# Kernel tuning notes

Hardware: AMD Instinct MI355X
Metric: run time of the kernel (lower is better)

## Reference

```python
import jax, jax.numpy as jnp
import numpy as np
import math

N, D = 4096, 1024

def setup_inputs() -> dict:
    key = jax.random.key(0)
    ks = jax.random.split(key, 12)
    x = jax.random.normal(ks[0], (N, D), dtype=jnp.float32)
    attention_mask = jax.random.randint(ks[1], (N, N), 0, 2).astype(jnp.float32)
    learnable_mask = jax.random.randint(ks[2], (N, N), 0, 2).astype(jnp.float32)
    boundary_mask = jax.random.randint(ks[3], (N, 1), 0, 2).astype(jnp.float32)
    s = 1.0 / math.sqrt(D)
    W_q = jax.random.normal(ks[4], (D, D), dtype=jnp.float32) * s
    b_q = jax.random.normal(ks[5], (D,), dtype=jnp.float32) * s
    W_k = jax.random.normal(ks[6], (D, D), dtype=jnp.float32) * s
    b_k = jax.random.normal(ks[7], (D,), dtype=jnp.float32) * s
    W_v = jax.random.normal(ks[8], (D, D), dtype=jnp.float32) * s
    b_v = jax.random.normal(ks[9], (D,), dtype=jnp.float32) * s
    connection = jax.random.normal(ks[10], (D, D), dtype=jnp.float32) * s
    bias = jnp.ones((1,), dtype=jnp.float32) * 0.01
    return {"x": x, "attention_mask": attention_mask, "learnable_mask": learnable_mask,
            "boundary_mask": boundary_mask, "W_q": W_q, "b_q": b_q, "W_k": W_k, "b_k": b_k,
            "W_v": W_v, "b_v": b_v, "connection": connection, "bias": bias}

def reference(x, attention_mask, learnable_mask, boundary_mask,
              W_q, b_q, W_k, b_k, W_v, b_v, connection, bias):
    # Linear layers (torch Linear: x @ W.T + b)
    q = x @ W_q.T + b_q            # [N, D]
    k = x @ W_k.T + b_k            # [N, D]
    v = x @ W_v.T + b_v            # [N, D]
    d_head = k.shape[-1]
    attention_logits = (q @ k.T) / jnp.sqrt(jnp.asarray(d_head, x.dtype))  # [N, N]
    connection_logits = (q @ connection) @ k.T + bias                      # [N, N]
    # straight-through hard sigmoid mask
    soft_mask = jax.nn.sigmoid(connection_logits)
    st_mask = (soft_mask > 0.5).astype(x.dtype) - jax.lax.stop_gradient(soft_mask) + soft_mask
    lm = st_mask * learnable_mask
    mask = attention_mask + lm
    mask = -10000.0 * (1.0 - mask)
    attention = jax.nn.softmax(attention_logits + mask, axis=-1)  # [N, N]
    x_residual = attention @ v                                    # [N, D]
    out = boundary_mask * x_residual + (1.0 - boundary_mask) * x
    return out
```

## Files before the change

### kernel.cpp

```cpp
#include <hip/hip_runtime.h>
#include <cstdint>


typedef __attribute__((ext_vector_type(8))) short short8;
typedef __attribute__((ext_vector_type(4))) float f32x4;
typedef __attribute__((ext_vector_type(4))) float f4v;
typedef __attribute__((ext_vector_type(4))) unsigned short u16x4;
typedef __attribute__((ext_vector_type(8))) unsigned short u16x8;

typedef unsigned short u16;
typedef unsigned char u8;

__device__ __forceinline__ u16 f2bf(float f) {
  unsigned u = __float_as_uint(f);
  u += 0x7fffu + ((u >> 16) & 1u);
  return (u16)(u >> 16);
}
__device__ __forceinline__ float bf2f(u16 h) {
  return __uint_as_float(((unsigned)h) << 16);
}

__device__ __forceinline__ void gld16(void* lds, const void* g) {
  __builtin_amdgcn_global_load_lds(
      (__attribute__((address_space(1))) void*)g,
      (__attribute__((address_space(3))) void*)lds,
      16, 0, 0);
}


__global__ void prep_x(const float* __restrict__ x, u16* __restrict__ xs3) {
  int id = blockIdx.x * 256 + threadIdx.x;
  int flat = id * 4;
  int n = flat >> 10, i = flat & 1023;
  f4v v = *(const f4v*)(x + (size_t)flat);
  u16x4 hi, lo;
#pragma unroll
  for (int e = 0; e < 4; e++) {
    float f = v[e];
    u16 h = f2bf(f);
    hi[e] = h;
    lo[e] = f2bf(f - bf2f(h));
  }
  size_t base = (size_t)n * 3072 + i;
  *(u16x4*)(xs3 + base) = hi;
  *(u16x4*)(xs3 + base + 1024) = lo;
  *(u16x4*)(xs3 + base + 2048) = hi;
}

__global__ void prep_w(const float* __restrict__ Wq, const float* __restrict__ Wk,
                       const float* __restrict__ Wv, u16* __restrict__ W3) {
  int id = blockIdx.x * 256 + threadIdx.x;
  int flat = id * 4;
  int o = flat >> 10, i = flat & 1023;
  const float* src = (o < 1024) ? (Wq + (size_t)o * 1024)
                   : (o < 2048) ? (Wk + (size_t)(o - 1024) * 1024)
                                : (Wv + (size_t)(o - 2048) * 1024);
  f4v v = *(const f4v*)(src + i);
  u16x4 hi, lo;
#pragma unroll
  for (int e = 0; e < 4; e++) {
    u16 h = f2bf(v[e]);
    hi[e] = h;
    lo[e] = f2bf(v[e] - bf2f(h));
  }
  size_t base = (size_t)o * 3072 + i;
  *(u16x4*)(W3 + base) = hi;
  *(u16x4*)(W3 + base + 1024) = hi;
  *(u16x4*)(W3 + base + 2048) = lo;
}

__global__ void prep_bias(const float* __restrict__ bq, const float* __restrict__ bk,
                          const float* __restrict__ bv, float* __restrict__ bp) {
  int id = blockIdx.x * 256 + threadIdx.x;
  float v = (id < 1024) ? bq[id] : (id < 2048) ? bk[id - 1024] : bv[id - 2048];
  bp[id] = v;
}

__global__ void prep_c(const float* __restrict__ C, u16* __restrict__ C3) {
  __shared__ float t[32][33];
  int lx = threadIdx.x & 31, ly = threadIdx.x >> 5;
  int i0 = blockIdx.x * 32, j0 = blockIdx.y * 32;
#pragma unroll
  for (int r = 0; r < 32; r += 8)
    t[ly + r][lx] = C[(size_t)(i0 + ly + r) * 1024 + j0 + lx];
  __syncthreads();
#pragma unroll
  for (int r = 0; r < 32; r += 8) {
    float f = t[lx][ly + r];
    u16 h = f2bf(f);
    u16 l = f2bf(f - bf2f(h));
    size_t o = (size_t)(j0 + ly + r) * 3072 + i0 + lx;
    C3[o] = h;
    C3[o + 1024] = h;
    C3[o + 2048] = l;
  }
}


struct EpiG1 {
  const float* bp; u16* qs3; u16* k3; u16* vt; int mode;
  __device__ void operator()(int r, int c, float v) const {
    if (mode == 0) {
      v += bp[c];
      u16 h = f2bf(v);
      u16 l = f2bf(v - bf2f(h));
      if (c < 1024) {
        size_t b = (size_t)r * 3072 + c;
        qs3[b] = h; qs3[b + 1024] = l; qs3[b + 2048] = h;
      } else {
        size_t b = (size_t)r * 3072 + (c - 1024);
        k3[b] = h; k3[b + 1024] = h; k3[b + 2048] = l;
      }
    } else {
      v += bp[2048 + r];
      vt[(size_t)r * 4096 + c] = f2bf(v);
    }
  }
};

struct EpiQCS {
  u16* qc3; u16* Sc; int isS;
  __device__ void operator()(int r, int c, float v) const {
    if (isS) {
      Sc[(size_t)r * 4096 + c] = f2bf(v);
    } else {
      u16 h = f2bf(v);
      u16 l = f2bf(v - bf2f(h));
      size_t b = (size_t)r * 3072 + c;
      qc3[b] = h; qc3[b + 1024] = l; qc3[b + 2048] = h;
    }
  }
};

struct EpiCL {
  u8* st; float b0;
  __device__ void operator()(int r, int c, float v) const {
    st[(size_t)r * 4096 + c] = (v + b0 > 0.f) ? 1 : 0;
  }
};

struct EpiPart {
  float* part;
  __device__ void operator()(int r, int c, float v) const {
    part[(size_t)r * 1024 + c] = v;
  }
};

template <class Epi>
__device__ __forceinline__ void gemm_core(
    const u16* __restrict__ A, const u16* __restrict__ B,
    int lda, int ldb, int K, int mBase, int nBase, Epi epi) {
  __shared__ __align__(16) u16 lA[128 * 64];
  __shared__ __align__(16) u16 lB[128 * 64];
  const int tid = threadIdx.x;
  const int wave = tid >> 6, lane = tid & 63;
  const int wm = wave & 1, wn = wave >> 1;
  const int lane16 = lane & 15, quad = lane >> 4;

  const int srow = tid >> 3;
  const int gchunk = ((tid & 7) ^ (srow & 7)) * 8;
  const u16* aP = A + (size_t)(mBase + srow) * lda + gchunk;
  const u16* bP = B + (size_t)(nBase + srow) * ldb + gchunk;
  const int woff = wave * 1024;

  const int rsw = lane16 & 7;
  const u16* raB = lA + (wm * 64 + lane16) * 64;
  const u16* rbB = lB + (wn * 64 + lane16) * 64;

  f32x4 acc[4][4];
#pragma unroll
  for (int i = 0; i < 4; i++)
#pragma unroll
    for (int j = 0; j < 4; j++) acc[i][j] = (f32x4){0.f, 0.f, 0.f, 0.f};

  for (int k0 = 0; k0 < K; k0 += 64) {
#pragma unroll
    for (int i = 0; i < 4; i++) {
      gld16((char*)lA + i * 4096 + woff, aP + (size_t)(32 * i) * lda + k0);
      gld16((char*)lB + i * 4096 + woff, bP + (size_t)(32 * i) * ldb + k0);
    }
    __syncthreads();
    short8 af[2][4], bfr[2][4];
#pragma unroll
    for (int s = 0; s < 2; s++) {
      const int sl = (((s << 2) + quad) ^ rsw) * 8;
#pragma unroll
      for (int j = 0; j < 4; j++) {
        af[s][j]  = *(const short8*)(raB + j * 1024 + sl);
        bfr[s][j] = *(const short8*)(rbB + j * 1024 + sl);
      }
    }
#pragma unroll
    for (int s = 0; s < 2; s++)
#pragma unroll
      for (int im = 0; im < 4; im++)
#pragma unroll
        for (int in = 0; in < 4; in++)
          acc[im][in] = __builtin_amdgcn_mfma_f32_16x16x32_bf16(
              af[s][im], bfr[s][in], acc[im][in], 0, 0, 0);
    __syncthreads();
  }

#pragma unroll
  for (int im = 0; im < 4; im++)
#pragma unroll
    for (int in = 0; in < 4; in++)
#pragma unroll
      for (int i = 0; i < 4; i++) {
        int r = mBase + wm * 64 + im * 16 + quad * 4 + i;
        int c = nBase + wn * 64 + in * 16 + lane16;
        epi(r, c, acc[im][in][i]);
      }
}

__global__ __launch_bounds__(256, 2) void gemm_g1(
    const u16* __restrict__ xs3, const u16* __restrict__ W3,
    const float* __restrict__ bp, u16* __restrict__ qs3,
    u16* __restrict__ k3, u16* __restrict__ vt) {
  const int bid = blockIdx.x;
  if (bid < 512) {
    gemm_core(xs3, W3, 3072, 3072, 3072, (bid >> 4) * 128, (bid & 15) * 128,
              EpiG1{bp, qs3, k3, vt, 0});
  } else {
    const int t = bid - 512;
    gemm_core(W3 + (size_t)2048 * 3072, xs3, 3072, 3072, 1024,
              (t & 7) * 128, (t >> 3) * 128, EpiG1{bp, qs3, k3, vt, 1});
  }
}

__global__ __launch_bounds__(256, 2) void gemm_qc_s(
    const u16* __restrict__ qs3, const u16* __restrict__ C3,
    const u16* __restrict__ k3, u16* __restrict__ qc3, u16* __restrict__ Sc) {
  const int bid = blockIdx.x;
  if (bid < 256) {
    gemm_core(qs3, C3, 3072, 3072, 3072, (bid >> 3) * 128, (bid & 7) * 128,
              EpiQCS{qc3, Sc, 0});
  } else {
    const int t = bid - 256;
    gemm_core(qs3, k3, 3072, 3072, 1024, (t >> 5) * 128, (t & 31) * 128,
              EpiQCS{qc3, Sc, 1});
  }
}

__global__ __launch_bounds__(256, 2) void gemm_cl(
    const u16* __restrict__ qc3, const u16* __restrict__ k3,
    const float* __restrict__ bias, u8* __restrict__ st) {
  gemm_core(qc3, k3, 3072, 3072, 3072, blockIdx.y * 128, blockIdx.x * 128,
            EpiCL{st, bias[0]});
}

__global__ __launch_bounds__(256, 2) void gemm_pv(
    const u16* __restrict__ P, const u16* __restrict__ vt,
    float* __restrict__ parts) {
  const size_t kOff = (size_t)blockIdx.z * 2048;
  gemm_core(P + kOff, vt + kOff, 4096, 4096, 2048,
            blockIdx.y * 128, blockIdx.x * 128,
            EpiPart{parts + (size_t)blockIdx.z * 4096 * 1024});
}

__global__ void reduce_out(const float* __restrict__ x, const float* __restrict__ bm,
                           const float* __restrict__ parts, float* __restrict__ out) {
  int id = blockIdx.x * 256 + threadIdx.x;
  int flat = id * 4;
  int r = flat >> 10;
  float b = bm[r];
  f4v xv = *(const f4v*)(x + (size_t)flat);
  f4v p0 = *(const f4v*)(parts + (size_t)flat);
  f4v p1 = *(const f4v*)(parts + (size_t)4096 * 1024 + flat);
  f4v o;
#pragma unroll
  for (int e = 0; e < 4; e++) o[e] = b * (p0[e] + p1[e]) + (1.0f - b) * xv[e];
  *(f4v*)(out + (size_t)flat) = o;
}

__global__ __launch_bounds__(256) void mask_softmax(
    const u16* __restrict__ Sc, const u8* __restrict__ st,
    const float* __restrict__ am, const float* __restrict__ lm,
    u16* __restrict__ P) {
  const int n = blockIdx.x, tid = threadIdx.x;
  const int lane = tid & 63, wave = tid >> 6;
  const u16* Srow = Sc + (size_t)n * 4096;
  const u8* Trow = st + (size_t)n * 4096;
  const float* Arow = am + (size_t)n * 4096;
  const float* Lrow = lm + (size_t)n * 4096;

  float lg[16];
  float mx = -3.4e38f;
#pragma unroll
  for (int j = 0; j < 2; j++) {
    int base = (tid + 256 * j) * 8;
    u16x8 s8 = *(const u16x8*)(Srow + base);
    unsigned long long t8 = *(const unsigned long long*)(Trow + base);
    f4v a0 = *(const f4v*)(Arow + base), a1 = *(const f4v*)(Arow + base + 4);
    f4v l0 = *(const f4v*)(Lrow + base), l1 = *(const f4v*)(Lrow + base + 4);
#pragma unroll
    for (int e = 0; e < 8; e++) {
      float stv = ((t8 >> (8 * e)) & 1ull) ? 1.f : 0.f;
      float a = (e < 4) ? a0[e] : a1[e - 4];
      float l = (e < 4) ? l0[e] : l1[e - 4];
      float mv = a + stv * l;
      float v = bf2f(s8[e]) * 0.03125f - 10000.f * (1.f - mv);
      lg[j * 8 + e] = v;
      mx = fmaxf(mx, v);
    }
  }
#pragma unroll
  for (int o = 32; o; o >>= 1) mx = fmaxf(mx, __shfl_xor(mx, o));
  __shared__ float smax[4], ssum[4];
  if (lane == 0) smax[wave] = mx;
  __syncthreads();
  mx = fmaxf(fmaxf(smax[0], smax[1]), fmaxf(smax[2], smax[3]));

  float sum = 0.f;
#pragma unroll
  for (int i = 0; i < 16; i++) { lg[i] = __expf(lg[i] - mx); sum += lg[i]; }
#pragma unroll
  for (int o = 32; o; o >>= 1) sum += __shfl_xor(sum, o);
  if (lane == 0) ssum[wave] = sum;
  __syncthreads();
  float inv = 1.f / (ssum[0] + ssum[1] + ssum[2] + ssum[3]);

  u16* Pr = P + (size_t)n * 4096;
#pragma unroll
  for (int j = 0; j < 2; j++) {
    int base = (tid + 256 * j) * 8;
    u16x8 o8;
#pragma unroll
    for (int e = 0; e < 8; e++) o8[e] = f2bf(lg[j * 8 + e] * inv);
    *(u16x8*)(Pr + base) = o8;
  }
}


extern "C" void kernel_launch(void* const* d_in, const int* in_sizes, int n_in,
                              void* d_out, int out_size, void* d_ws, size_t ws_size,
                              hipStream_t stream) {
  const float* x    = (const float*)d_in[0];
  const float* am   = (const float*)d_in[1];
  const float* lm   = (const float*)d_in[2];
  const float* bm   = (const float*)d_in[3];
  const float* Wq   = (const float*)d_in[4];
  const float* bq   = (const float*)d_in[5];
  const float* Wk   = (const float*)d_in[6];
  const float* bk   = (const float*)d_in[7];
  const float* Wv   = (const float*)d_in[8];
  const float* bv   = (const float*)d_in[9];
  const float* Cc   = (const float*)d_in[10];
  const float* bias = (const float*)d_in[11];
  float* out = (float*)d_out;
  char* ws = (char*)d_ws;

  if (ws_size < 0xB010000) return;

  u16*  xs3 = (u16*) (ws + 0x0000000);
  u16*  W3  = (u16*) (ws + 0x1800000);
  u16*  C3  = (u16*) (ws + 0x2A00000);
  float* bp = (float*)(ws + 0x3000000);
  u16*  qs3 = (u16*) (ws + 0x3010000);
  u16*  qc3 = (u16*) (ws + 0x4810000);
  u16*  k3  = (u16*) (ws + 0x6010000);
  u16*  vt  = (u16*) (ws + 0x7810000);
  u16*  Sc  = (u16*) (ws + 0x8010000);
  u8*   st  = (u8*)  (ws + 0xA010000);
  u16*  P   = (u16*) (ws + 0x0000000);
  float* parts = (float*)(ws + 0x4810000);

  prep_x   <<<4096, 256, 0, stream>>>(x, xs3);
  prep_w   <<<3072, 256, 0, stream>>>(Wq, Wk, Wv, W3);
  prep_bias<<<12,   256, 0, stream>>>(bq, bk, bv, bp);
  prep_c   <<<dim3(32, 32), 256, 0, stream>>>(Cc, C3);

  gemm_g1<<<768, 256, 0, stream>>>(xs3, W3, bp, qs3, k3, vt);
  gemm_qc_s<<<1280, 256, 0, stream>>>(qs3, C3, k3, qc3, Sc);
  gemm_cl<<<dim3(32, 32), 256, 0, stream>>>(qc3, k3, bias, st);
  mask_softmax<<<4096, 256, 0, stream>>>(Sc, st, am, lm, P);
  gemm_pv<<<dim3(8, 32, 2), 256, 0, stream>>>(P, vt, parts);
  reduce_out<<<4096, 256, 0, stream>>>(x, bm, parts, out);
}
```

Measured before the change: 486.9 us.

## Use 256x256 tile GEMM with 4-stage pipeline for connection-logit and PV GEMMs

Adds a 512-thread GEMM core with 256x256 output tiles, a 4-deep LDS ring buffer and explicit waitcnt/barrier scheduling, and uses it for the connection-logits GEMM and the attention-times-V GEMM. The goal is more operand reuse per byte loaded and better overlap of global loads with MFMA work. Block indices are remapped for cache locality. The PV GEMM is split-K into four parts so it still fills the device, which means reduce_out now sums four fp32 partials and moves more memory. The larger tile uses more LDS and registers per block, which may cut occupancy.

```diff
diff --git a/kernel.cpp b/kernel.cpp
--- a/kernel.cpp
+++ b/kernel.cpp
@@ -213,6 +213,111 @@
       }
 }
 
+
+template <class Epi>
+__device__ __forceinline__ void gemm256_core(
+    const u16* __restrict__ A, const u16* __restrict__ B,
+    int lda, int ldb, int K, int mBase, int nBase, Epi epi) {
+  __shared__ __align__(16) u16 lA[4][256 * 32];
+  __shared__ __align__(16) u16 lB[4][256 * 32];
+  const int tid  = threadIdx.x;
+  const int wave = tid >> 6, lane = tid & 63;
+  const int lane16 = lane & 15, quad = lane >> 4;
+  const int wm = wave >> 2, wn = wave & 3;
+  const int NT = K >> 5;
+
+  const int srow = tid >> 2;
+  const int gch  = ((tid & 3) ^ ((tid >> 3) & 3)) * 8;
+  const u16* aS = A + (size_t)(mBase + srow) * lda + gch;
+  const u16* bS = B + (size_t)(nBase + srow) * ldb + gch;
+  const size_t aStep = (size_t)128 * lda, bStep = (size_t)128 * ldb;
+  const int ldsW = wave * 1024;
+
+  const int sw   = (lane16 >> 1) & 3;
+  const int aOff = (wm * 128 + lane16) * 64 + ((quad ^ sw) * 16);
+  const int bOff = (wn * 64  + lane16) * 64 + ((quad ^ sw) * 16);
+
+  f32x4 acc[8][4];
+#pragma unroll
+  for (int j = 0; j < 8; j++)
+#pragma unroll
+    for (int n = 0; n < 4; n++) acc[j][n] = (f32x4){0.f, 0.f, 0.f, 0.f};
+
+  short8 af[8], bfr[4];
+
+  auto stage = [&](int t) {
+    const int bb = (t & 3) * 16384;
+    const size_t kk = (size_t)(t << 5);
+#pragma unroll
+    for (int i = 0; i < 2; i++) {
+      gld16((char*)lA + bb + i * 8192 + ldsW, aS + (size_t)i * aStep + kk);
+      gld16((char*)lB + bb + i * 8192 + ldsW, bS + (size_t)i * bStep + kk);
+    }
+  };
+  auto rdfrags = [&](int t) {
+    const char* la = (const char*)lA + (t & 3) * 16384 + aOff;
+    const char* lb = (const char*)lB + (t & 3) * 16384 + bOff;
+#pragma unroll
+    for (int j = 0; j < 8; j++) af[j] = *(const short8*)(la + j * 1024);
+#pragma unroll
+    for (int n = 0; n < 4; n++) bfr[n] = *(const short8*)(lb + n * 1024);
+  };
+  auto mfma32 = [&]() {
+    __builtin_amdgcn_s_setprio(1);
+#pragma unroll
+    for (int j = 0; j < 8; j++)
+#pragma unroll
+      for (int n = 0; n < 4; n++)
+        acc[j][n] = __builtin_amdgcn_mfma_f32_16x16x32_bf16(
+            af[j], bfr[n], acc[j][n], 0, 0, 0);
+    __builtin_amdgcn_s_setprio(0);
+  };
+
+  stage(0); stage(1); stage(2);
+  asm volatile("s_waitcnt vmcnt(8)" ::: "memory");
+  __builtin_amdgcn_sched_barrier(0);
+  __builtin_amdgcn_s_barrier();
+  __builtin_amdgcn_sched_barrier(0);
+
+  int t = 0;
+  for (; t + 4 <= NT; ++t) {
+    rdfrags(t);
+    stage(t + 3);
+    asm volatile("s_waitcnt vmcnt(8) lgkmcnt(0)" ::: "memory");
+    __builtin_amdgcn_sched_barrier(0);
+    __builtin_amdgcn_s_barrier();
+    __builtin_amdgcn_sched_barrier(0);
+    mfma32();
+  }
+  rdfrags(t);
+  asm volatile("s_waitcnt vmcnt(4) lgkmcnt(0)" ::: "memory");
+  __builtin_amdgcn_sched_barrier(0);
+  __builtin_amdgcn_s_barrier();
+  __builtin_amdgcn_sched_barrier(0);
+  mfma32();
+  ++t;
+  rdfrags(t);
+  asm volatile("s_waitcnt vmcnt(0) lgkmcnt(0)" ::: "memory");
+  __builtin_amdgcn_sched_barrier(0);
+  __builtin_amdgcn_s_barrier();
+  __builtin_amdgcn_sched_barrier(0);
+  mfma32();
+  ++t;
+  rdfrags(t);
+  asm volatile("s_waitcnt lgkmcnt(0)" ::: "memory");
+  __builtin_amdgcn_sched_barrier(0);
+  mfma32();
+
+#pragma unroll
+  for (int j = 0; j < 8; j++)
+#pragma unroll
+    for (int n = 0; n < 4; n++)
+#pragma unroll
+      for (int i = 0; i < 4; i++)
+        epi(mBase + wm * 128 + j * 16 + quad * 4 + i,
+            nBase + wn * 64 + n * 16 + lane16, acc[j][n][i]);
+}
+
 __global__ __launch_bounds__(256, 2) void gemm_g1(
     const u16* __restrict__ xs3, const u16* __restrict__ W3,
     const float* __restrict__ bp, u16* __restrict__ qs3,
@@ -242,34 +347,43 @@
   }
 }
 
-__global__ __launch_bounds__(256, 2) void gemm_cl(
+__global__ __launch_bounds__(512, 2) void gemm_cl256(
     const u16* __restrict__ qc3, const u16* __restrict__ k3,
     const float* __restrict__ bias, u8* __restrict__ st) {
-  gemm_core(qc3, k3, 3072, 3072, 3072, blockIdx.y * 128, blockIdx.x * 128,
-            EpiCL{st, bias[0]});
-}
-
-__global__ __launch_bounds__(256, 2) void gemm_pv(
+  const int bid = blockIdx.x;
+  const int wg = (bid & 7) * 32 + (bid >> 3);
+  gemm256_core(qc3, k3, 3072, 3072, 3072, (wg >> 4) * 256, (wg & 15) * 256,
+               EpiCL{st, bias[0]});
+}
+
+__global__ __launch_bounds__(512, 2) void gemm_pv256(
     const u16* __restrict__ P, const u16* __restrict__ vt,
-    float* __restrict__ parts) {
-  const size_t kOff = (size_t)blockIdx.z * 2048;
-  gemm_core(P + kOff, vt + kOff, 4096, 4096, 2048,
-            blockIdx.y * 128, blockIdx.x * 128,
-            EpiPart{parts + (size_t)blockIdx.z * 4096 * 1024});
+    float* __restrict__ p01, float* __restrict__ p23) {
+  const int bid = blockIdx.x;
+  const int z = bid >> 6, rem = bid & 63;
+  float* base = ((z < 2) ? p01 : p23) + (size_t)(z & 1) * (4096ull * 1024ull);
+  const size_t kOff = (size_t)z * 1024;
+  gemm256_core(P + kOff, vt + kOff, 4096, 4096, 1024,
+               (rem >> 2) * 256, (rem & 3) * 256, EpiPart{base});
 }
 
 __global__ void reduce_out(const float* __restrict__ x, const float* __restrict__ bm,
-                           const float* __restrict__ parts, float* __restrict__ out) {
+                           const float* __restrict__ p01, const float* __restrict__ p23,
+                           float* __restrict__ out) {
   int id = blockIdx.x * 256 + threadIdx.x;
   int flat = id * 4;
   int r = flat >> 10;
   float b = bm[r];
+  const size_t SL = (size_t)4096 * 1024;
   f4v xv = *(const f4v*)(x + (size_t)flat);
-  f4v p0 = *(const f4v*)(parts + (size_t)flat);
-  f4v p1 = *(const f4v*)(parts + (size_t)4096 * 1024 + flat);
+  f4v a0 = *(const f4v*)(p01 + (size_t)flat);
+  f4v a1 = *(const f4v*)(p01 + SL + flat);
+  f4v a2 = *(const f4v*)(p23 + (size_t)flat);
+  f4v a3 = *(const f4v*)(p23 + SL + flat);
   f4v o;
 #pragma unroll
-  for (int e = 0; e < 4; e++) o[e] = b * (p0[e] + p1[e]) + (1.0f - b) * xv[e];
+  for (int e = 0; e < 4; e++)
+    o[e] = b * ((a0[e] + a1[e]) + (a2[e] + a3[e])) + (1.0f - b) * xv[e];
   *(f4v*)(out + (size_t)flat) = o;
 }
 
@@ -363,7 +477,8 @@
   u16*  Sc  = (u16*) (ws + 0x8010000);
   u8*   st  = (u8*)  (ws + 0xA010000);
   u16*  P   = (u16*) (ws + 0x0000000);
-  float* parts = (float*)(ws + 0x4810000);
+  float* parts01 = (float*)(ws + 0x4810000);
+  float* parts23 = (float*)(ws + 0x8010000);
 
   prep_x   <<<4096, 256, 0, stream>>>(x, xs3);
   prep_w   <<<3072, 256, 0, stream>>>(Wq, Wk, Wv, W3);
@@ -372,8 +487,8 @@
 
   gemm_g1<<<768, 256, 0, stream>>>(xs3, W3, bp, qs3, k3, vt);
   gemm_qc_s<<<1280, 256, 0, stream>>>(qs3, C3, k3, qc3, Sc);
-  gemm_cl<<<dim3(32, 32), 256, 0, stream>>>(qc3, k3, bias, st);
+  gemm_cl256<<<256, 512, 0, stream>>>(qc3, k3, bias, st);
   mask_softmax<<<4096, 256, 0, stream>>>(Sc, st, am, lm, P);
-  gemm_pv<<<dim3(8, 32, 2), 256, 0, stream>>>(P, vt, parts);
-  reduce_out<<<4096, 256, 0, stream>>>(x, bm, parts, out);
-}
+  gemm_pv256<<<256, 512, 0, stream>>>(P, vt, parts01, parts23);
+  reduce_out<<<4096, 256, 0, stream>>>(x, bm, parts01, parts23, out);
+}
```

New measurement: 471.9 us. 3.1% less time.

## Compact query rows by boundary mask and skip attention for masked-out rows

Applied to the files above, without the earlier changes.

Adds a prefix-scan kernel that collects the row indices where boundary_mask is nonzero. The Q projection, QC/S GEMMs, connection-logit GEMM, softmax and PV GEMM then run only over these compacted rows, and tiles past the count exit early. Rows with a zero mask copy x directly in the final kernel. The PV split-K also goes from two to four slices to keep enough blocks in flight, at the cost of more partial buffers and a single-block scan kernel in front.

```diff
diff --git a/kernel.cpp b/kernel.cpp
--- a/kernel.cpp
+++ b/kernel.cpp
@@ -27,6 +27,32 @@
       16, 0, 0);
 }
 
+
+__global__ void prep_bm(const float* __restrict__ bm, int* __restrict__ idx,
+                        int* __restrict__ cntp) {
+  __shared__ int ps[1024];
+  const int t = threadIdx.x;
+  int loc[4];
+  int c = 0;
+#pragma unroll
+  for (int e = 0; e < 4; e++) {
+    int r = t * 4 + e;
+    if (bm[r] != 0.0f) loc[c++] = r;
+  }
+  ps[t] = c;
+  __syncthreads();
+  for (int off = 1; off < 1024; off <<= 1) {
+    int v = (t >= off) ? ps[t - off] : 0;
+    __syncthreads();
+    ps[t] += v;
+    __syncthreads();
+  }
+  int base = ps[t] - c;
+  for (int i = 0; i < c; i++) idx[base + i] = loc[i];
+  int cnt = ps[1023];
+  if (t == 0) cntp[0] = cnt;
+  for (int r = cnt + t; r < 4096; r += 1024) idx[r] = 0;
+}
 
 __global__ void prep_x(const float* __restrict__ x, u16* __restrict__ xs3) {
   int id = blockIdx.x * 256 + threadIdx.x;
@@ -97,24 +123,33 @@
 }
 
 
-struct EpiG1 {
-  const float* bp; u16* qs3; u16* k3; u16* vt; int mode;
-  __device__ void operator()(int r, int c, float v) const {
-    if (mode == 0) {
-      v += bp[c];
-      u16 h = f2bf(v);
-      u16 l = f2bf(v - bf2f(h));
-      if (c < 1024) {
-        size_t b = (size_t)r * 3072 + c;
-        qs3[b] = h; qs3[b + 1024] = l; qs3[b + 2048] = h;
-      } else {
-        size_t b = (size_t)r * 3072 + (c - 1024);
-        k3[b] = h; k3[b + 1024] = h; k3[b + 2048] = l;
-      }
-    } else {
-      v += bp[2048 + r];
-      vt[(size_t)r * 4096 + c] = f2bf(v);
-    }
+struct EpiQ {
+  const float* bp; u16* qs3;
+  __device__ void operator()(int r, int c, float v) const {
+    v += bp[c];
+    u16 h = f2bf(v);
+    u16 l = f2bf(v - bf2f(h));
+    size_t b = (size_t)r * 3072 + c;
+    qs3[b] = h; qs3[b + 1024] = l; qs3[b + 2048] = h;
+  }
+};
+
+struct EpiK {
+  const float* bp; u16* k3;
+  __device__ void operator()(int r, int c, float v) const {
+    v += bp[1024 + c];
+    u16 h = f2bf(v);
+    u16 l = f2bf(v - bf2f(h));
+    size_t b = (size_t)r * 3072 + c;
+    k3[b] = h; k3[b + 1024] = h; k3[b + 2048] = l;
+  }
+};
+
+struct EpiVt {
+  const float* bp; u16* vt;
+  __device__ void operator()(int r, int c, float v) const {
+    v += bp[2048 + r];
+    vt[(size_t)r * 4096 + c] = f2bf(v);
   }
 };
 
@@ -140,16 +175,17 @@
 };
 
 struct EpiPart {
-  float* part;
-  __device__ void operator()(int r, int c, float v) const {
-    part[(size_t)r * 1024 + c] = v;
+  float* part; const int* idx; int cnt;
+  __device__ void operator()(int r, int c, float v) const {
+    if (r < cnt) part[(size_t)idx[r] * 1024 + c] = v;
   }
 };
 
 template <class Epi>
 __device__ __forceinline__ void gemm_core(
     const u16* __restrict__ A, const u16* __restrict__ B,
-    int lda, int ldb, int K, int mBase, int nBase, Epi epi) {
+    int lda, int ldb, int K, int mBase, int nBase,
+    const int* __restrict__ ridx, Epi epi) {
   __shared__ __align__(16) u16 lA[128 * 64];
   __shared__ __align__(16) u16 lB[128 * 64];
   const int tid = threadIdx.x;
@@ -159,7 +195,13 @@
 
   const int srow = tid >> 3;
   const int gchunk = ((tid & 7) ^ (srow & 7)) * 8;
-  const u16* aP = A + (size_t)(mBase + srow) * lda + gchunk;
+  const u16* aPi[4];
+#pragma unroll
+  for (int i = 0; i < 4; i++) {
+    int row = mBase + srow + 32 * i;
+    int g = ridx ? ridx[row] : row;
+    aPi[i] = A + (size_t)g * lda + gchunk;
+  }
   const u16* bP = B + (size_t)(nBase + srow) * ldb + gchunk;
   const int woff = wave * 1024;
 
@@ -176,7 +218,7 @@
   for (int k0 = 0; k0 < K; k0 += 64) {
 #pragma unroll
     for (int i = 0; i < 4; i++) {
-      gld16((char*)lA + i * 4096 + woff, aP + (size_t)(32 * i) * lda + k0);
+      gld16((char*)lA + i * 4096 + woff, aPi[i] + k0);
       gld16((char*)lB + i * 4096 + woff, bP + (size_t)(32 * i) * ldb + k0);
     }
     __syncthreads();
@@ -216,73 +258,108 @@
 __global__ __launch_bounds__(256, 2) void gemm_g1(
     const u16* __restrict__ xs3, const u16* __restrict__ W3,
     const float* __restrict__ bp, u16* __restrict__ qs3,
-    u16* __restrict__ k3, u16* __restrict__ vt) {
+    u16* __restrict__ k3, u16* __restrict__ vt,
+    const int* __restrict__ idx, const int* __restrict__ cntp) {
   const int bid = blockIdx.x;
-  if (bid < 512) {
-    gemm_core(xs3, W3, 3072, 3072, 3072, (bid >> 4) * 128, (bid & 15) * 128,
-              EpiG1{bp, qs3, k3, vt, 0});
+  if (bid < 256) {
+    gemm_core(xs3, W3 + (size_t)1024 * 3072, 3072, 3072, 3072,
+              (bid >> 3) * 128, (bid & 7) * 128, nullptr, EpiK{bp, k3});
+  } else if (bid < 512) {
+    const int t = bid - 256;
+    const int mBase = (t >> 3) * 128;
+    if (mBase >= cntp[0]) return;
+    gemm_core(xs3, W3, 3072, 3072, 3072, mBase, (t & 7) * 128, idx,
+              EpiQ{bp, qs3});
   } else {
     const int t = bid - 512;
     gemm_core(W3 + (size_t)2048 * 3072, xs3, 3072, 3072, 1024,
-              (t & 7) * 128, (t >> 3) * 128, EpiG1{bp, qs3, k3, vt, 1});
+              (t & 7) * 128, (t >> 3) * 128, nullptr, EpiVt{bp, vt});
   }
 }
 
 __global__ __launch_bounds__(256, 2) void gemm_qc_s(
     const u16* __restrict__ qs3, const u16* __restrict__ C3,
-    const u16* __restrict__ k3, u16* __restrict__ qc3, u16* __restrict__ Sc) {
+    const u16* __restrict__ k3, u16* __restrict__ qc3, u16* __restrict__ Sc,
+    const int* __restrict__ cntp) {
   const int bid = blockIdx.x;
+  const int cnt = cntp[0];
   if (bid < 256) {
-    gemm_core(qs3, C3, 3072, 3072, 3072, (bid >> 3) * 128, (bid & 7) * 128,
+    const int mBase = (bid >> 3) * 128;
+    if (mBase >= cnt) return;
+    gemm_core(qs3, C3, 3072, 3072, 3072, mBase, (bid & 7) * 128, nullptr,
               EpiQCS{qc3, Sc, 0});
   } else {
     const int t = bid - 256;
-    gemm_core(qs3, k3, 3072, 3072, 1024, (t >> 5) * 128, (t & 31) * 128,
+    const int mBase = (t >> 5) * 128;
+    if (mBase >= cnt) return;
+    gemm_core(qs3, k3, 3072, 3072, 1024, mBase, (t & 31) * 128, nullptr,
               EpiQCS{qc3, Sc, 1});
   }
 }
 
 __global__ __launch_bounds__(256, 2) void gemm_cl(
     const u16* __restrict__ qc3, const u16* __restrict__ k3,
-    const float* __restrict__ bias, u8* __restrict__ st) {
-  gemm_core(qc3, k3, 3072, 3072, 3072, blockIdx.y * 128, blockIdx.x * 128,
+    const float* __restrict__ bias, u8* __restrict__ st,
+    const int* __restrict__ cntp) {
+  const int bid = blockIdx.x;
+  const int mBase = (bid >> 5) * 128;
+  if (mBase >= cntp[0]) return;
+  gemm_core(qc3, k3, 3072, 3072, 3072, mBase, (bid & 31) * 128, nullptr,
             EpiCL{st, bias[0]});
 }
 
 __global__ __launch_bounds__(256, 2) void gemm_pv(
     const u16* __restrict__ P, const u16* __restrict__ vt,
-    float* __restrict__ parts) {
-  const size_t kOff = (size_t)blockIdx.z * 2048;
-  gemm_core(P + kOff, vt + kOff, 4096, 4096, 2048,
-            blockIdx.y * 128, blockIdx.x * 128,
-            EpiPart{parts + (size_t)blockIdx.z * 4096 * 1024});
+    float* __restrict__ p01, float* __restrict__ p23,
+    const int* __restrict__ idx, const int* __restrict__ cntp) {
+  const int bid = blockIdx.x;
+  const int z = bid >> 8, rem = bid & 255;
+  const int cnt = cntp[0];
+  const int mBase = (rem >> 3) * 128;
+  if (mBase >= cnt) return;
+  float* base = ((z < 2) ? p01 : p23) + (size_t)(z & 1) * (4096ull * 1024ull);
+  const size_t kOff = (size_t)z * 1024;
+  gemm_core(P + kOff, vt + kOff, 4096, 4096, 1024, mBase, (rem & 7) * 128,
+            nullptr, EpiPart{base, idx, cnt});
 }
 
 __global__ void reduce_out(const float* __restrict__ x, const float* __restrict__ bm,
-                           const float* __restrict__ parts, float* __restrict__ out) {
+                           const float* __restrict__ p01, const float* __restrict__ p23,
+                           float* __restrict__ out) {
   int id = blockIdx.x * 256 + threadIdx.x;
   int flat = id * 4;
   int r = flat >> 10;
   float b = bm[r];
   f4v xv = *(const f4v*)(x + (size_t)flat);
-  f4v p0 = *(const f4v*)(parts + (size_t)flat);
-  f4v p1 = *(const f4v*)(parts + (size_t)4096 * 1024 + flat);
   f4v o;
-#pragma unroll
-  for (int e = 0; e < 4; e++) o[e] = b * (p0[e] + p1[e]) + (1.0f - b) * xv[e];
+  if (b != 0.0f) {
+    const size_t SL = (size_t)4096 * 1024;
+    f4v a0 = *(const f4v*)(p01 + (size_t)flat);
+    f4v a1 = *(const f4v*)(p01 + SL + flat);
+    f4v a2 = *(const f4v*)(p23 + (size_t)flat);
+    f4v a3 = *(const f4v*)(p23 + SL + flat);
+#pragma unroll
+    for (int e = 0; e < 4; e++)
+      o[e] = b * ((a0[e] + a1[e]) + (a2[e] + a3[e])) + (1.0f - b) * xv[e];
+  } else {
+    o = xv;
+  }
   *(f4v*)(out + (size_t)flat) = o;
 }
 
 __global__ __launch_bounds__(256) void mask_softmax(
     const u16* __restrict__ Sc, const u8* __restrict__ st,
     const float* __restrict__ am, const float* __restrict__ lm,
-    u16* __restrict__ P) {
+    u16* __restrict__ P, const int* __restrict__ idx,
+    const int* __restrict__ cntp) {
   const int n = blockIdx.x, tid = threadIdx.x;
+  if (n >= cntp[0]) return;
+  const int orow = idx[n];
   const int lane = tid & 63, wave = tid >> 6;
   const u16* Srow = Sc + (size_t)n * 4096;
   const u8* Trow = st + (size_t)n * 4096;
-  const float* Arow = am + (size_t)n * 4096;
-  const float* Lrow = lm + (size_t)n * 4096;
+  const float* Arow = am + (size_t)orow * 4096;
+  const float* Lrow = lm + (size_t)orow * 4096;
 
   float lg[16];
   float mx = -3.4e38f;
@@ -356,6 +433,8 @@
   u16*  W3  = (u16*) (ws + 0x1800000);
   u16*  C3  = (u16*) (ws + 0x2A00000);
   float* bp = (float*)(ws + 0x3000000);
+  int*  idx = (int*)  (ws + 0x3004000);
+  int*  cnt = (int*)  (ws + 0x3008000);
   u16*  qs3 = (u16*) (ws + 0x3010000);
   u16*  qc3 = (u16*) (ws + 0x4810000);
   u16*  k3  = (u16*) (ws + 0x6010000);
@@ -363,17 +442,19 @@
   u16*  Sc  = (u16*) (ws + 0x8010000);
   u8*   st  = (u8*)  (ws + 0xA010000);
   u16*  P   = (u16*) (ws + 0x0000000);
-  float* parts = (float*)(ws + 0x4810000);
-
+  float* parts01 = (float*)(ws + 0x4810000);
+  float* parts23 = (float*)(ws + 0x8010000);
+
+  prep_bm  <<<1, 1024, 0, stream>>>(bm, idx, cnt);
   prep_x   <<<4096, 256, 0, stream>>>(x, xs3);
   prep_w   <<<3072, 256, 0, stream>>>(Wq, Wk, Wv, W3);
   prep_bias<<<12,   256, 0, stream>>>(bq, bk, bv, bp);
   prep_c   <<<dim3(32, 32), 256, 0, stream>>>(Cc, C3);
 
-  gemm_g1<<<768, 256, 0, stream>>>(xs3, W3, bp, qs3, k3, vt);
-  gemm_qc_s<<<1280, 256, 0, stream>>>(qs3, C3, k3, qc3, Sc);
-  gemm_cl<<<dim3(32, 32), 256, 0, stream>>>(qc3, k3, bias, st);
-  mask_softmax<<<4096, 256, 0, stream>>>(Sc, st, am, lm, P);
-  gemm_pv<<<dim3(8, 32, 2), 256, 0, stream>>>(P, vt, parts);
-  reduce_out<<<4096, 256, 0, stream>>>(x, bm, parts, out);
-}
+  gemm_g1<<<768, 256, 0, stream>>>(xs3, W3, bp, qs3, k3, vt, idx, cnt);
+  gemm_qc_s<<<1280, 256, 0, stream>>>(qs3, C3, k3, qc3, Sc, cnt);
+  gemm_cl<<<1024, 256, 0, stream>>>(qc3, k3, bias, st, cnt);
+  mask_softmax<<<4096, 256, 0, stream>>>(Sc, st, am, lm, P, idx, cnt);
+  gemm_pv<<<1024, 256, 0, stream>>>(P, vt, parts01, parts23, idx, cnt);
+  reduce_out<<<4096, 256, 0, stream>>>(x, bm, parts01, parts23, out);
+}
```

Measured after the change: 456.5 us. 6.2% less time.
